# Optimization experiments

Measured on AMD Instinct MI355X. Metric: run time of the kernel, lower is better.

Reference implementation:

```python
import jax, jax.numpy as jnp
import numpy as np


def _conv1x1_relu(x, w, b):
    # x: [B,C,T,H,W], w: [O,C], b: [O] -> 1x1x1 conv + ReLU
    y = jnp.einsum('oc,bcthw->bothw', w, x) + b[None, :, None, None, None]
    return jax.nn.relu(y)


def _maxpool3d_2(x):
    # MaxPool3d(kernel=2, stride=2, padding=0) over T,H,W
    return jax.lax.reduce_window(
        x, -jnp.inf, jax.lax.max,
        window_dimensions=(1, 1, 2, 2, 2),
        window_strides=(1, 1, 2, 2, 2),
        padding='VALID')


def setup_inputs() -> dict:
    key = jax.random.key(0)
    ks = jax.random.split(key, 10)
    B, C, T, H, W = 4, 128, 16, 32, 32
    C1, C2 = 4, 2
    d1, d2 = C // C1, C // C2  # 32, 64
    s = 0.05
    return {
        'x':  jax.random.normal(ks[0], (B, C, T, H, W), dtype=jnp.float32),
        'wf': jax.random.normal(ks[1], (d1, C), dtype=jnp.float32) * s,
        'bf': jnp.zeros((d1,), dtype=jnp.float32),
        'wg': jax.random.normal(ks[2], (d1, C), dtype=jnp.float32) * s,
        'bg': jnp.zeros((d1,), dtype=jnp.float32),
        'wh': jax.random.normal(ks[3], (d2, C), dtype=jnp.float32) * s,
        'bh': jnp.zeros((d2,), dtype=jnp.float32),
        'wo': jax.random.normal(ks[4], (C, d2), dtype=jnp.float32) * s,
        'bo': jnp.zeros((C,), dtype=jnp.float32),
        'gamma': jnp.asarray([0.5], dtype=jnp.float32),
    }


def reference(x, wf, bf, wg, bg, wh, bh, wo, bo, gamma):
    B, C, T, H, W = x.shape
    N = T * H * W
    theta = _conv1x1_relu(x, wf, bf).reshape(B, wf.shape[0], N)          # [B,d1,N]
    phi = _maxpool3d_2(_conv1x1_relu(x, wg, bg)).reshape(B, wg.shape[0], N // 8)  # [B,d1,M]
    g = _maxpool3d_2(_conv1x1_relu(x, wh, bh)).reshape(B, wh.shape[0], N // 8)    # [B,d2,M]
    # attn = softmax(theta^T @ phi) over keys (no 1/sqrt(d) scaling, as in source)
    scores = jnp.einsum('bcn,bcm->bnm', theta, phi)                      # [B,N,M]
    attn = jax.nn.softmax(scores, axis=-1)
    attn_g = jnp.einsum('bcm,bnm->bcn', g, attn).reshape(B, wh.shape[0], T, H, W)
    out = x + gamma[0] * _conv1x1_relu(attn_g, wo, bo)
    return out
```

## Files before the change

kernel.cpp:

```cpp
#include <hip/hip_runtime.h>
#include <hip/hip_bf16.h>

#define NB 4
#define NC 128
#define NN 16384
#define NM 2048

typedef __attribute__((ext_vector_type(8))) short bf16x8;
typedef __attribute__((ext_vector_type(4))) float f32x4;
typedef __attribute__((ext_vector_type(4))) unsigned short u16x4;
typedef __attribute__((ext_vector_type(2))) unsigned int u32x2;
typedef unsigned short us;

#define MFMA16(a,b,c) __builtin_amdgcn_mfma_f32_16x16x32_bf16((a),(b),(c),0,0,0)

__device__ __forceinline__ us f2bf(float f){
  unsigned int u = __float_as_uint(f);
  u += 0x7fffu + ((u >> 16) & 1u);
  return (us)(u >> 16);
}
__device__ __forceinline__ float bf2f(us h){
  return __uint_as_float(((unsigned int)h) << 16);
}
__device__ __forceinline__ unsigned int packbf2(float lo, float hi){
  return (__float_as_uint(hi) & 0xffff0000u) | (__float_as_uint(lo) >> 16);
}

__global__ void k0_prep(const float* __restrict__ wf, const float* __restrict__ wg,
                        const float* __restrict__ wh, const float* __restrict__ bfp,
                        const float* __restrict__ bgp, const float* __restrict__ bhp,
                        const float* __restrict__ wo,
                        us* __restrict__ Wcat, us* __restrict__ wob,
                        float* __restrict__ bcat){
  int i = blockIdx.x * 256 + threadIdx.x;
  if (i < 16384){
    int o = i >> 7, c = i & 127;
    float v = (o < 32) ? wf[o*128 + c] : (o < 64) ? wg[(o-32)*128 + c] : wh[(o-64)*128 + c];
    Wcat[i] = f2bf(v);
  } else if (i < 24576){
    wob[i - 16384] = f2bf(wo[i - 16384]);
  } else if (i < 24704){
    int k = i - 24576;
    bcat[k] = (k < 32) ? bfp[k] : (k < 64) ? bgp[k-32] : bhp[k-64];
  }
}

__global__ __launch_bounds__(256, 4) void k2_conv(
    const float* __restrict__ x, const us* __restrict__ Wcat,
    const float* __restrict__ bcat,
    us* __restrict__ thetaT, us* __restrict__ Ywh){
  __shared__ __align__(16) us xtile[64*136];
  __shared__ __align__(16) us theta_sh[64*40];
  __shared__ us Ytmp[96*33];
  int blk = blockIdx.x;
  int b = blk >> 8, nblk = blk & 255;
  int n0 = nblk * 64;
  int tid = threadIdx.x;

  {
    int nbase = (tid & 15) * 4;
    int c0 = (tid >> 4) * 8;
    float va[8][4];
    #pragma unroll
    for (int j = 0; j < 8; ++j){
      float4 v = *(const float4*)(x + ((size_t)(b*128 + c0 + j)) * NN + n0 + nbase);
      va[j][0]=v.x; va[j][1]=v.y; va[j][2]=v.z; va[j][3]=v.w;
    }
    #pragma unroll
    for (int nn = 0; nn < 4; ++nn){
      bf16x8 r;
      #pragma unroll
      for (int j = 0; j < 8; ++j) r[j] = (short)f2bf(va[j][nn]);
      *(bf16x8*)&xtile[(nbase+nn)*136 + c0] = r;
    }
  }
  __syncthreads();

  int lane = tid & 63, w = tid >> 6;
  int ln = lane & 15, gq = lane >> 4;
  bf16x8 xf[4];
  #pragma unroll
  for (int kf = 0; kf < 4; ++kf)
    xf[kf] = *(const bf16x8*)&xtile[(w*16+ln)*136 + kf*32 + gq*8];

  #pragma unroll
  for (int ot = 0; ot < 8; ++ot){
    f32x4 acc = {0.f,0.f,0.f,0.f};
    #pragma unroll
    for (int kf = 0; kf < 4; ++kf){
      bf16x8 wfr = *(const bf16x8*)(Wcat + (ot*16 + ln)*128 + kf*32 + gq*8);
      acc = MFMA16(wfr, xf[kf], acc);
    }
    float y[4];
    #pragma unroll
    for (int i = 0; i < 4; ++i){
      int o = ot*16 + gq*4 + i;
      float v = acc[i] + bcat[o];
      y[i] = v > 0.f ? v : 0.f;
    }
    if (ot < 2){
      u16x4 pk;
      #pragma unroll
      for (int i = 0; i < 4; ++i) pk[i] = f2bf(y[i]);
      *(u16x4*)&theta_sh[(w*16+ln)*40 + ot*16 + gq*4] = pk;
    } else {
      #pragma unroll
      for (int i = 0; i < 4; ++i){
        float ym = fmaxf(y[i], __shfl_xor(y[i], 1));
        if ((ln & 1) == 0){
          int r = ot*16 + gq*4 + i - 32;
          Ytmp[r*33 + ((w*16 + ln) >> 1)] = f2bf(ym);
        }
      }
    }
  }
  __syncthreads();

  {
    int row = tid >> 2, coff = (tid & 3) * 8;
    bf16x8 tv = *(const bf16x8*)&theta_sh[row*40 + coff];
    *(bf16x8*)(thetaT + ((size_t)b*NN + n0 + row)*32 + coff) = tv;
  }
  int tt = n0 >> 10;
  int h2 = nblk & 15;
  #pragma unroll
  for (int q = 0; q < 6; ++q){
    int idx = q*256 + tid;
    int r = idx >> 4, j = idx & 15;
    us a = Ytmp[r*33 + j], bsh = Ytmp[r*33 + j + 16];
    us v = a > bsh ? a : bsh;
    Ywh[(((size_t)(b*96 + r))*16 + tt)*256 + h2*16 + j] = v;
  }
}

__global__ void k3_pool(const us* __restrict__ Ywh,
                        us* __restrict__ phiT, us* __restrict__ g_){
  __shared__ us trans[64][36];
  int blk = blockIdx.x;
  int t = threadIdx.x;
  if (blk < 128){
    int b = blk >> 5, mseg = blk & 31;
    int m0 = mseg * 64;
    int u = m0 >> 8, p0 = m0 & 255;
    int c = t >> 3, mj = t & 7;
    const us* r0 = Ywh + (((size_t)(b*96 + c))*16 + 2*u)*256 + p0 + mj*8;
    const us* r1 = r0 + 256;
    #pragma unroll
    for (int k = 0; k < 8; ++k){
      us a = r0[k], bsh = r1[k];
      trans[mj*8 + k][c] = a > bsh ? a : bsh;
    }
    __syncthreads();
    int ml = t >> 2, cg = t & 3;
    u16x4 o0, o1;
    #pragma unroll
    for (int k = 0; k < 4; ++k){ o0[k] = trans[ml][cg*8 + k]; o1[k] = trans[ml][cg*8 + 4 + k]; }
    *(u16x4*)(phiT + ((size_t)b*NM + m0 + ml)*32 + cg*8)     = o0;
    *(u16x4*)(phiT + ((size_t)b*NM + m0 + ml)*32 + cg*8 + 4) = o1;
  } else {
    int blk2 = blk - 128;
    int b = blk2 >> 6, c2 = blk2 & 63;
    int u = t >> 5, p = (t & 31) * 8;
    const us* r0 = Ywh + (((size_t)(b*96 + 32 + c2))*16 + 2*u)*256 + p;
    const us* r1 = r0 + 256;
    u16x4 o0, o1;
    #pragma unroll
    for (int k = 0; k < 4; ++k){
      us a0 = r0[k],   b0 = r1[k];
      us a1 = r0[4+k], b1 = r1[4+k];
      o0[k] = a0 > b0 ? a0 : b0;
      o1[k] = a1 > b1 ? a1 : b1;
    }
    *(u16x4*)(g_ + ((size_t)(b*64 + c2))*NM + t*8)     = o0;
    *(u16x4*)(g_ + ((size_t)(b*64 + c2))*NM + t*8 + 4) = o1;
  }
}

__global__ __launch_bounds__(256, 4) void k4_attn(
    const us* __restrict__ thetaT, const us* __restrict__ phiT,
    const us* __restrict__ g_, us* __restrict__ pacc,
    float* __restrict__ lsumA){
  __shared__ __align__(16) us phi_lds[2][32][40];
  __shared__ __align__(16) us g_lds[2][64][40];
  __shared__ __align__(16) us P_lds[4][16][40];

  int bx = blockIdx.x;
  int b = bx >> 8, qb = (bx >> 1) & 127, kh = bx & 1;
  int tid = threadIdx.x;
  int lane = tid & 63, wv = tid >> 6;
  int ln = lane & 15, gq = lane >> 4;
  int nq = qb*128 + wv*32;
  int ch0 = kh * 32;

  const us* thb = thetaT + (size_t)b*NN*32;
  const us* phb = phiT   + (size_t)b*NM*32;
  const us* gb  = g_     + (size_t)b*64*NM;

  bf16x8 thf0 = *(const bf16x8*)(thb + (size_t)(nq + ln)*32 + gq*8);
  bf16x8 thf1 = *(const bf16x8*)(thb + (size_t)(nq + 16 + ln)*32 + gq*8);

  f32x4 acc[2][4];
  #pragma unroll
  for (int q = 0; q < 2; ++q)
    #pragma unroll
    for (int c2t = 0; c2t < 4; ++c2t) acc[q][c2t] = (f32x4){0.f,0.f,0.f,0.f};
  float lsum0 = 0.f, lsum1 = 0.f;

  int gr = tid >> 2, gp = tid & 3;
  const us* sgp_g = gb + (size_t)gr*NM + ch0*32 + gp*8;
  us* slg0 = &g_lds[0][gr][gp*8];
  us* slg1 = &g_lds[1][gr][gp*8];
  bool hasphi = tid < 128;
  int pr = (tid >> 2) & 31, pp = tid & 3;
  const us* sgp_p = phb + ((size_t)(ch0*32 + pr))*32 + pp*8;
  us* slp0 = &phi_lds[0][pr][pp*8];
  us* slp1 = &phi_lds[1][pr][pp*8];

  { bf16x8 srg = *(const bf16x8*)(sgp_g); *(bf16x8*)slg0 = srg; }
  if (hasphi){ bf16x8 srp = *(const bf16x8*)(sgp_p); *(bf16x8*)slp0 = srp; }
  __syncthreads();

  bf16x8 srg_n = {}, srp_n = {};
  for (int lc = 0; lc < 32; ++lc){
    int cur = lc & 1;
    if (lc + 1 < 32){
      srg_n = *(const bf16x8*)(sgp_g + (size_t)(lc+1)*32);
      if (hasphi) srp_n = *(const bf16x8*)(sgp_p + (size_t)(lc+1)*1024);
    }
    bf16x8 pf0 = *(const bf16x8*)(&phi_lds[cur][ln][gq*8]);
    bf16x8 pf1 = *(const bf16x8*)(&phi_lds[cur][16+ln][gq*8]);
    bf16x8 gf0 = *(const bf16x8*)(&g_lds[cur][ln][gq*8]);
    bf16x8 gf1 = *(const bf16x8*)(&g_lds[cur][16+ln][gq*8]);
    bf16x8 gf2 = *(const bf16x8*)(&g_lds[cur][32+ln][gq*8]);
    bf16x8 gf3 = *(const bf16x8*)(&g_lds[cur][48+ln][gq*8]);
    f32x4 z = {0.f,0.f,0.f,0.f};

    {
      f32x4 s0 = MFMA16(pf0, thf0, z);
      f32x4 s1 = MFMA16(pf1, thf0, z);
      float p0[4], p1[4];
      #pragma unroll
      for (int i = 0; i < 4; ++i){ p0[i] = __expf(s0[i]); p1[i] = __expf(s1[i]); }
      lsum0 += ((p0[0]+p0[1]) + (p0[2]+p0[3])) + ((p1[0]+p1[1]) + (p1[2]+p1[3]));
      u32x2 w0 = { packbf2(p0[0],p0[1]), packbf2(p0[2],p0[3]) };
      u32x2 w1 = { packbf2(p1[0],p1[1]), packbf2(p1[2],p1[3]) };
      *(u32x2*)(&P_lds[wv][ln][gq*4])      = w0;
      *(u32x2*)(&P_lds[wv][ln][16+gq*4])   = w1;
      bf16x8 paf = *(const bf16x8*)(&P_lds[wv][ln][gq*8]);
      acc[0][0] = MFMA16(paf, gf0, acc[0][0]);
      acc[0][1] = MFMA16(paf, gf1, acc[0][1]);
      acc[0][2] = MFMA16(paf, gf2, acc[0][2]);
      acc[0][3] = MFMA16(paf, gf3, acc[0][3]);
    }
    {
      f32x4 s0 = MFMA16(pf0, thf1, z);
      f32x4 s1 = MFMA16(pf1, thf1, z);
      float p0[4], p1[4];
      #pragma unroll
      for (int i = 0; i < 4; ++i){ p0[i] = __expf(s0[i]); p1[i] = __expf(s1[i]); }
      lsum1 += ((p0[0]+p0[1]) + (p0[2]+p0[3])) + ((p1[0]+p1[1]) + (p1[2]+p1[3]));
      u32x2 w0 = { packbf2(p0[0],p0[1]), packbf2(p0[2],p0[3]) };
      u32x2 w1 = { packbf2(p1[0],p1[1]), packbf2(p1[2],p1[3]) };
      *(u32x2*)(&P_lds[wv][ln][gq*4])      = w0;
      *(u32x2*)(&P_lds[wv][ln][16+gq*4])   = w1;
      bf16x8 paf = *(const bf16x8*)(&P_lds[wv][ln][gq*8]);
      acc[1][0] = MFMA16(paf, gf0, acc[1][0]);
      acc[1][1] = MFMA16(paf, gf1, acc[1][1]);
      acc[1][2] = MFMA16(paf, gf2, acc[1][2]);
      acc[1][3] = MFMA16(paf, gf3, acc[1][3]);
    }
    if (lc + 1 < 32){
      *(bf16x8*)(((lc+1)&1) ? slg1 : slg0) = srg_n;
      if (hasphi) *(bf16x8*)(((lc+1)&1) ? slp1 : slp0) = srp_n;
    }
    __syncthreads();
  }

  lsum0 += __shfl_xor(lsum0, 16); lsum0 += __shfl_xor(lsum0, 32);
  lsum1 += __shfl_xor(lsum1, 16); lsum1 += __shfl_xor(lsum1, 32);

  us* pb = pacc + ((size_t)(kh*NB + b))*NN*64;
  #pragma unroll
  for (int i = 0; i < 4; ++i){
    int r0 = nq + gq*4 + i, r1 = nq + 16 + gq*4 + i;
    #pragma unroll
    for (int c2t = 0; c2t < 4; ++c2t){
      pb[(size_t)r0*64 + c2t*16 + ln] = f2bf(acc[0][c2t][i]);
      pb[(size_t)r1*64 + c2t*16 + ln] = f2bf(acc[1][c2t][i]);
    }
  }
  size_t lbase = ((size_t)(kh*NB + b))*NN;
  if (gq == 0)      lsumA[lbase + nq + ln]      = lsum0;
  else if (gq == 1) lsumA[lbase + nq + 16 + ln] = lsum1;
}

__device__ __forceinline__ bf16x8 combine8(bf16x8 a, bf16x8 b, float inv){
  bf16x8 r;
  #pragma unroll
  for (int k = 0; k < 8; ++k){
    float f = (bf2f((us)a[k]) + bf2f((us)b[k])) * inv;
    r[k] = (short)f2bf(f);
  }
  return r;
}

__global__ __launch_bounds__(256, 4) void k5_out(
    const float* __restrict__ x, const us* __restrict__ pacc,
    const float* __restrict__ lsumA,
    const us* __restrict__ wob, const float* __restrict__ bo,
    const float* __restrict__ gamma, float* __restrict__ out){
  __shared__ __align__(16) float vt[128*68];
  int blk = blockIdx.x;
  int b = blk >> 8, nblk = blk & 255;
  int n0 = nblk * 64;
  int tid = threadIdx.x;
  int lane = tid & 63, w = tid >> 6;
  int ln = lane & 15, gq = lane >> 4;
  int n = n0 + w*16 + ln;
  int nl = w*16 + ln;

  const us* p0 = pacc + ((size_t)b*NN + n)*64;
  const us* p1 = pacc + ((size_t)(NB + b)*NN + n)*64;
  float l = lsumA[(size_t)b*NN + n] + lsumA[(size_t)(NB + b)*NN + n];
  float inv = 1.0f / l;
  bf16x8 a0lo = *(const bf16x8*)(p0 + gq*8);
  bf16x8 a1lo = *(const bf16x8*)(p1 + gq*8);
  bf16x8 a0hi = *(const bf16x8*)(p0 + 32 + gq*8);
  bf16x8 a1hi = *(const bf16x8*)(p1 + 32 + gq*8);
  bf16x8 bfr0 = combine8(a0lo, a1lo, inv);
  bf16x8 bfr1 = combine8(a0hi, a1hi, inv);

  float gam = gamma[0];
  #pragma unroll
  for (int ot = 0; ot < 8; ++ot){
    f32x4 acc = {0.f,0.f,0.f,0.f};
    bf16x8 a0 = *(const bf16x8*)(wob + (ot*16 + ln)*64 + gq*8);
    bf16x8 a1 = *(const bf16x8*)(wob + (ot*16 + ln)*64 + 32 + gq*8);
    acc = MFMA16(a0, bfr0, acc);
    acc = MFMA16(a1, bfr1, acc);
    #pragma unroll
    for (int i = 0; i < 4; ++i){
      int o = ot*16 + gq*4 + i;
      float v = acc[i] + bo[o];
      v = v > 0.f ? v : 0.f;
      vt[o*68 + nl] = gam * v;
    }
  }
  __syncthreads();

  int o = tid >> 1, half = tid & 1;
  const float* xr = x + ((size_t)b*128 + o)*NN + n0 + half*32;
  float* outr = out + ((size_t)b*128 + o)*NN + n0 + half*32;
  const float* vr = &vt[o*68 + half*32];
  #pragma unroll
  for (int k = 0; k < 8; ++k){
    float4 xv = *(const float4*)(xr + k*4);
    float4 dv = *(const float4*)(vr + k*4);
    float4 ov = { xv.x + dv.x, xv.y + dv.y, xv.z + dv.z, xv.w + dv.w };
    *(float4*)(outr + k*4) = ov;
  }
}

extern "C" void kernel_launch(void* const* d_in, const int* in_sizes, int n_in,
                              void* d_out, int out_size, void* d_ws, size_t ws_size,
                              hipStream_t stream){
  const float* x   = (const float*)d_in[0];
  const float* wf  = (const float*)d_in[1];
  const float* bfp = (const float*)d_in[2];
  const float* wg  = (const float*)d_in[3];
  const float* bgp = (const float*)d_in[4];
  const float* wh  = (const float*)d_in[5];
  const float* bhp = (const float*)d_in[6];
  const float* wo  = (const float*)d_in[7];
  const float* bo  = (const float*)d_in[8];
  const float* gam = (const float*)d_in[9];
  float* out = (float*)d_out;
  char* ws = (char*)d_ws;

  const size_t OFF_WCAT = 0;
  const size_t OFF_WO   = 32768;
  const size_t OFF_BCAT = 49152;
  const size_t OFF_TH   = 65536;
  const size_t OFF_YWH  = OFF_TH  + (size_t)NB*NN*32*2;
  const size_t OFF_PHI  = OFF_YWH + (size_t)NB*96*16*256*2;
  const size_t OFF_G    = OFF_PHI + (size_t)NB*NM*32*2;
  const size_t OFF_PACC = OFF_G   + (size_t)NB*64*NM*2;
  const size_t OFF_LSUM = OFF_PACC+ (size_t)2*NB*NN*64*2;

  us*    Wcat    = (us*)(ws + OFF_WCAT);
  us*    wob     = (us*)(ws + OFF_WO);
  float* bcat    = (float*)(ws + OFF_BCAT);
  us*    thetaT  = (us*)(ws + OFF_TH);
  us*    Ywh     = (us*)(ws + OFF_YWH);
  us*    phiT    = (us*)(ws + OFF_PHI);
  us*    g_      = (us*)(ws + OFF_G);
  us*    pacc    = (us*)(ws + OFF_PACC);
  float* lsumA   = (float*)(ws + OFF_LSUM);

  k0_prep<<<97, 256, 0, stream>>>(wf, wg, wh, bfp, bgp, bhp, wo, Wcat, wob, bcat);
  k2_conv<<<1024, 256, 0, stream>>>(x, Wcat, bcat, thetaT, Ywh);
  k3_pool<<<384, 256, 0, stream>>>(Ywh, phiT, g_);
  k4_attn<<<1024, 256, 0, stream>>>(thetaT, phiT, g_, pacc, lsumA);
  k5_out<<<1024, 256, 0, stream>>>(x, pacc, lsumA, wob, bo, gam, out);
}
```

Baseline: 176.7 us.

## Fuse attention and output projection, drop key split and partial buffers

Merges the attention kernel and the output 1x1-conv/residual kernel into one. Each block now walks all keys instead of half of them, so the bf16 partial accumulators and partial softmax sums no longer go through global memory and the combine step disappears. Normalization, the output projection MFMA, bias, ReLU and the residual add are done in-register with a small LDS staging buffer. In exchange the grid is halved to 512 blocks with a longer serial loop (launch bounds lowered to 2), and the final x/out accesses are strided per lane rather than float4-coalesced.

```diff
diff --git a/kernel.cpp b/kernel.cpp
--- a/kernel.cpp
+++ b/kernel.cpp
@@ -176,21 +176,22 @@
   }
 }
 
-__global__ __launch_bounds__(256, 4) void k4_attn(
+__global__ __launch_bounds__(256, 2) void k4_attn_out(
     const us* __restrict__ thetaT, const us* __restrict__ phiT,
-    const us* __restrict__ g_, us* __restrict__ pacc,
-    float* __restrict__ lsumA){
-  __shared__ __align__(16) us phi_lds[2][32][40];
-  __shared__ __align__(16) us g_lds[2][64][40];
-  __shared__ __align__(16) us P_lds[4][16][40];
+    const us* __restrict__ g_, const us* __restrict__ wob,
+    const float* __restrict__ bo, const float* __restrict__ gamma,
+    const float* __restrict__ x, float* __restrict__ out){
+  __shared__ __align__(16) us smem[10240];
+  us* phi_lds = smem;
+  us* g_lds   = smem + 2560;
+  us* P_lds   = smem + 7680;
 
   int bx = blockIdx.x;
-  int b = bx >> 8, qb = (bx >> 1) & 127, kh = bx & 1;
+  int b = bx >> 7, qb = bx & 127;
   int tid = threadIdx.x;
   int lane = tid & 63, wv = tid >> 6;
   int ln = lane & 15, gq = lane >> 4;
   int nq = qb*128 + wv*32;
-  int ch0 = kh * 32;
 
   const us* thb = thetaT + (size_t)b*NN*32;
   const us* phb = phiT   + (size_t)b*NM*32;
@@ -207,32 +208,32 @@
   float lsum0 = 0.f, lsum1 = 0.f;
 
   int gr = tid >> 2, gp = tid & 3;
-  const us* sgp_g = gb + (size_t)gr*NM + ch0*32 + gp*8;
-  us* slg0 = &g_lds[0][gr][gp*8];
-  us* slg1 = &g_lds[1][gr][gp*8];
+  const us* sgp_g = gb + (size_t)gr*NM + gp*8;
+  us* slg0 = &g_lds[0*2560 + gr*40 + gp*8];
+  us* slg1 = &g_lds[1*2560 + gr*40 + gp*8];
   bool hasphi = tid < 128;
   int pr = (tid >> 2) & 31, pp = tid & 3;
-  const us* sgp_p = phb + ((size_t)(ch0*32 + pr))*32 + pp*8;
-  us* slp0 = &phi_lds[0][pr][pp*8];
-  us* slp1 = &phi_lds[1][pr][pp*8];
+  const us* sgp_p = phb + (size_t)pr*32 + pp*8;
+  us* slp0 = &phi_lds[0*1280 + pr*40 + pp*8];
+  us* slp1 = &phi_lds[1*1280 + pr*40 + pp*8];
 
   { bf16x8 srg = *(const bf16x8*)(sgp_g); *(bf16x8*)slg0 = srg; }
   if (hasphi){ bf16x8 srp = *(const bf16x8*)(sgp_p); *(bf16x8*)slp0 = srp; }
   __syncthreads();
 
   bf16x8 srg_n = {}, srp_n = {};
-  for (int lc = 0; lc < 32; ++lc){
+  for (int lc = 0; lc < 64; ++lc){
     int cur = lc & 1;
-    if (lc + 1 < 32){
+    if (lc + 1 < 64){
       srg_n = *(const bf16x8*)(sgp_g + (size_t)(lc+1)*32);
       if (hasphi) srp_n = *(const bf16x8*)(sgp_p + (size_t)(lc+1)*1024);
     }
-    bf16x8 pf0 = *(const bf16x8*)(&phi_lds[cur][ln][gq*8]);
-    bf16x8 pf1 = *(const bf16x8*)(&phi_lds[cur][16+ln][gq*8]);
-    bf16x8 gf0 = *(const bf16x8*)(&g_lds[cur][ln][gq*8]);
-    bf16x8 gf1 = *(const bf16x8*)(&g_lds[cur][16+ln][gq*8]);
-    bf16x8 gf2 = *(const bf16x8*)(&g_lds[cur][32+ln][gq*8]);
-    bf16x8 gf3 = *(const bf16x8*)(&g_lds[cur][48+ln][gq*8]);
+    bf16x8 pf0 = *(const bf16x8*)(&phi_lds[cur*1280 + ln*40 + gq*8]);
+    bf16x8 pf1 = *(const bf16x8*)(&phi_lds[cur*1280 + (16+ln)*40 + gq*8]);
+    bf16x8 gf0 = *(const bf16x8*)(&g_lds[cur*2560 + ln*40 + gq*8]);
+    bf16x8 gf1 = *(const bf16x8*)(&g_lds[cur*2560 + (16+ln)*40 + gq*8]);
+    bf16x8 gf2 = *(const bf16x8*)(&g_lds[cur*2560 + (32+ln)*40 + gq*8]);
+    bf16x8 gf3 = *(const bf16x8*)(&g_lds[cur*2560 + (48+ln)*40 + gq*8]);
     f32x4 z = {0.f,0.f,0.f,0.f};
 
     {
@@ -244,9 +245,9 @@
       lsum0 += ((p0[0]+p0[1]) + (p0[2]+p0[3])) + ((p1[0]+p1[1]) + (p1[2]+p1[3]));
       u32x2 w0 = { packbf2(p0[0],p0[1]), packbf2(p0[2],p0[3]) };
       u32x2 w1 = { packbf2(p1[0],p1[1]), packbf2(p1[2],p1[3]) };
-      *(u32x2*)(&P_lds[wv][ln][gq*4])      = w0;
-      *(u32x2*)(&P_lds[wv][ln][16+gq*4])   = w1;
-      bf16x8 paf = *(const bf16x8*)(&P_lds[wv][ln][gq*8]);
+      *(u32x2*)(&P_lds[wv*640 + ln*40 + gq*4])      = w0;
+      *(u32x2*)(&P_lds[wv*640 + ln*40 + 16 + gq*4]) = w1;
+      bf16x8 paf = *(const bf16x8*)(&P_lds[wv*640 + ln*40 + gq*8]);
       acc[0][0] = MFMA16(paf, gf0, acc[0][0]);
       acc[0][1] = MFMA16(paf, gf1, acc[0][1]);
       acc[0][2] = MFMA16(paf, gf2, acc[0][2]);
@@ -261,15 +262,15 @@
       lsum1 += ((p0[0]+p0[1]) + (p0[2]+p0[3])) + ((p1[0]+p1[1]) + (p1[2]+p1[3]));
       u32x2 w0 = { packbf2(p0[0],p0[1]), packbf2(p0[2],p0[3]) };
       u32x2 w1 = { packbf2(p1[0],p1[1]), packbf2(p1[2],p1[3]) };
-      *(u32x2*)(&P_lds[wv][ln][gq*4])      = w0;
-      *(u32x2*)(&P_lds[wv][ln][16+gq*4])   = w1;
-      bf16x8 paf = *(const bf16x8*)(&P_lds[wv][ln][gq*8]);
+      *(u32x2*)(&P_lds[wv*640 + ln*40 + gq*4])      = w0;
+      *(u32x2*)(&P_lds[wv*640 + ln*40 + 16 + gq*4]) = w1;
+      bf16x8 paf = *(const bf16x8*)(&P_lds[wv*640 + ln*40 + gq*8]);
       acc[1][0] = MFMA16(paf, gf0, acc[1][0]);
       acc[1][1] = MFMA16(paf, gf1, acc[1][1]);
       acc[1][2] = MFMA16(paf, gf2, acc[1][2]);
       acc[1][3] = MFMA16(paf, gf3, acc[1][3]);
     }
-    if (lc + 1 < 32){
+    if (lc + 1 < 64){
       *(bf16x8*)(((lc+1)&1) ? slg1 : slg0) = srg_n;
       if (hasphi) *(bf16x8*)(((lc+1)&1) ? slp1 : slp0) = srp_n;
     }
@@ -279,85 +280,43 @@
   lsum0 += __shfl_xor(lsum0, 16); lsum0 += __shfl_xor(lsum0, 32);
   lsum1 += __shfl_xor(lsum1, 16); lsum1 += __shfl_xor(lsum1, 32);
 
-  us* pb = pacc + ((size_t)(kh*NB + b))*NN*64;
+  us* ag = smem + wv*2304;
+  float inv0[4], inv1[4];
   #pragma unroll
   for (int i = 0; i < 4; ++i){
-    int r0 = nq + gq*4 + i, r1 = nq + 16 + gq*4 + i;
-    #pragma unroll
-    for (int c2t = 0; c2t < 4; ++c2t){
-      pb[(size_t)r0*64 + c2t*16 + ln] = f2bf(acc[0][c2t][i]);
-      pb[(size_t)r1*64 + c2t*16 + ln] = f2bf(acc[1][c2t][i]);
-    }
-  }
-  size_t lbase = ((size_t)(kh*NB + b))*NN;
-  if (gq == 0)      lsumA[lbase + nq + ln]      = lsum0;
-  else if (gq == 1) lsumA[lbase + nq + 16 + ln] = lsum1;
-}
-
-__device__ __forceinline__ bf16x8 combine8(bf16x8 a, bf16x8 b, float inv){
-  bf16x8 r;
-  #pragma unroll
-  for (int k = 0; k < 8; ++k){
-    float f = (bf2f((us)a[k]) + bf2f((us)b[k])) * inv;
-    r[k] = (short)f2bf(f);
-  }
-  return r;
-}
-
-__global__ __launch_bounds__(256, 4) void k5_out(
-    const float* __restrict__ x, const us* __restrict__ pacc,
-    const float* __restrict__ lsumA,
-    const us* __restrict__ wob, const float* __restrict__ bo,
-    const float* __restrict__ gamma, float* __restrict__ out){
-  __shared__ __align__(16) float vt[128*68];
-  int blk = blockIdx.x;
-  int b = blk >> 8, nblk = blk & 255;
-  int n0 = nblk * 64;
-  int tid = threadIdx.x;
-  int lane = tid & 63, w = tid >> 6;
-  int ln = lane & 15, gq = lane >> 4;
-  int n = n0 + w*16 + ln;
-  int nl = w*16 + ln;
-
-  const us* p0 = pacc + ((size_t)b*NN + n)*64;
-  const us* p1 = pacc + ((size_t)(NB + b)*NN + n)*64;
-  float l = lsumA[(size_t)b*NN + n] + lsumA[(size_t)(NB + b)*NN + n];
-  float inv = 1.0f / l;
-  bf16x8 a0lo = *(const bf16x8*)(p0 + gq*8);
-  bf16x8 a1lo = *(const bf16x8*)(p1 + gq*8);
-  bf16x8 a0hi = *(const bf16x8*)(p0 + 32 + gq*8);
-  bf16x8 a1hi = *(const bf16x8*)(p1 + 32 + gq*8);
-  bf16x8 bfr0 = combine8(a0lo, a1lo, inv);
-  bf16x8 bfr1 = combine8(a0hi, a1hi, inv);
+    inv0[i] = 1.0f / __shfl(lsum0, gq*4 + i);
+    inv1[i] = 1.0f / __shfl(lsum1, gq*4 + i);
+  }
+  #pragma unroll
+  for (int c2t = 0; c2t < 4; ++c2t)
+    #pragma unroll
+    for (int i = 0; i < 4; ++i){
+      ag[(gq*4 + i)*72      + c2t*16 + ln] = f2bf(acc[0][c2t][i] * inv0[i]);
+      ag[(16 + gq*4 + i)*72 + c2t*16 + ln] = f2bf(acc[1][c2t][i] * inv1[i]);
+    }
 
   float gam = gamma[0];
   #pragma unroll
-  for (int ot = 0; ot < 8; ++ot){
-    f32x4 acc = {0.f,0.f,0.f,0.f};
-    bf16x8 a0 = *(const bf16x8*)(wob + (ot*16 + ln)*64 + gq*8);
-    bf16x8 a1 = *(const bf16x8*)(wob + (ot*16 + ln)*64 + 32 + gq*8);
-    acc = MFMA16(a0, bfr0, acc);
-    acc = MFMA16(a1, bfr1, acc);
-    #pragma unroll
-    for (int i = 0; i < 4; ++i){
-      int o = ot*16 + gq*4 + i;
-      float v = acc[i] + bo[o];
-      v = v > 0.f ? v : 0.f;
-      vt[o*68 + nl] = gam * v;
-    }
-  }
-  __syncthreads();
-
-  int o = tid >> 1, half = tid & 1;
-  const float* xr = x + ((size_t)b*128 + o)*NN + n0 + half*32;
-  float* outr = out + ((size_t)b*128 + o)*NN + n0 + half*32;
-  const float* vr = &vt[o*68 + half*32];
-  #pragma unroll
-  for (int k = 0; k < 8; ++k){
-    float4 xv = *(const float4*)(xr + k*4);
-    float4 dv = *(const float4*)(vr + k*4);
-    float4 ov = { xv.x + dv.x, xv.y + dv.y, xv.z + dv.z, xv.w + dv.w };
-    *(float4*)(outr + k*4) = ov;
+  for (int qt = 0; qt < 2; ++qt){
+    bf16x8 bfr0 = *(const bf16x8*)(&ag[(qt*16 + ln)*72 + gq*8]);
+    bf16x8 bfr1 = *(const bf16x8*)(&ag[(qt*16 + ln)*72 + 32 + gq*8]);
+    int n = nq + qt*16 + ln;
+    #pragma unroll
+    for (int ot = 0; ot < 8; ++ot){
+      f32x4 a2 = {0.f,0.f,0.f,0.f};
+      bf16x8 a0 = *(const bf16x8*)(wob + (ot*16 + ln)*64 + gq*8);
+      bf16x8 a1 = *(const bf16x8*)(wob + (ot*16 + ln)*64 + 32 + gq*8);
+      a2 = MFMA16(a0, bfr0, a2);
+      a2 = MFMA16(a1, bfr1, a2);
+      #pragma unroll
+      for (int i = 0; i < 4; ++i){
+        int o = ot*16 + gq*4 + i;
+        size_t idx = ((size_t)b*128 + o)*NN + n;
+        float v = a2[i] + bo[o];
+        v = v > 0.f ? v : 0.f;
+        out[idx] = x[idx] + gam * v;
+      }
+    }
   }
 }
 
@@ -384,8 +343,6 @@
   const size_t OFF_YWH  = OFF_TH  + (size_t)NB*NN*32*2;
   const size_t OFF_PHI  = OFF_YWH + (size_t)NB*96*16*256*2;
   const size_t OFF_G    = OFF_PHI + (size_t)NB*NM*32*2;
-  const size_t OFF_PACC = OFF_G   + (size_t)NB*64*NM*2;
-  const size_t OFF_LSUM = OFF_PACC+ (size_t)2*NB*NN*64*2;
 
   us*    Wcat    = (us*)(ws + OFF_WCAT);
   us*    wob     = (us*)(ws + OFF_WO);
@@ -394,12 +351,9 @@
   us*    Ywh     = (us*)(ws + OFF_YWH);
   us*    phiT    = (us*)(ws + OFF_PHI);
   us*    g_      = (us*)(ws + OFF_G);
-  us*    pacc    = (us*)(ws + OFF_PACC);
-  float* lsumA   = (float*)(ws + OFF_LSUM);
 
   k0_prep<<<97, 256, 0, stream>>>(wf, wg, wh, bfp, bgp, bhp, wo, Wcat, wob, bcat);
   k2_conv<<<1024, 256, 0, stream>>>(x, Wcat, bcat, thetaT, Ywh);
   k3_pool<<<384, 256, 0, stream>>>(Ywh, phiT, g_);
-  k4_attn<<<1024, 256, 0, stream>>>(thetaT, phiT, g_, pacc, lsumA);
-  k5_out<<<1024, 256, 0, stream>>>(x, pacc, lsumA, wob, bo, gam, out);
-}
+  k4_attn_out<<<512, 256, 0, stream>>>(thetaT, phiT, g_, wob, bo, gam, x, out);
+}
```

New measurement: 171.7 us. -2.8%, faster.
